# Performance work log

Hardware: AMD Instinct MI355X
Metric: run time of the kernel (lower is better)

The kernel has to match this reference:

```python
import jax, jax.numpy as jnp
import numpy as np

B, N, M, K = 2, 16384, 16384, 32
C_IN, C_OUT, KS = 64, 128, 15
RADIUS = 0.1
SIGMA = 0.5 * RADIUS  # module sets self.sigma = sigma * radius


def _generate_kernel_points(num_kpoints: int, radius: float) -> np.ndarray:
    # Fibonacci-sphere placement, matching the torch generate_kernel_points
    if num_kpoints == 1:
        return np.zeros((1, 3), dtype=np.float32)
    pts = np.zeros((num_kpoints, 3), dtype=np.float32)
    golden_angle = np.pi * (3 - np.sqrt(5))
    for i in range(num_kpoints):
        y = 1 - i / float(num_kpoints - 1) * 2
        r_y = np.sqrt(1 - y * y)
        theta = golden_angle * i
        pts[i] = np.array([np.cos(theta) * r_y, y, np.sin(theta) * r_y]) * radius
    return pts


def setup_inputs() -> dict:
    key = jax.random.key(0)
    k1, k2, k3, k4 = jax.random.split(key, 4)
    query_points = jax.random.uniform(k1, (B, N, 3), dtype=jnp.float32)
    support_points = jax.random.uniform(k2, (B, M, 3), dtype=jnp.float32)
    support_features = jax.random.normal(k3, (B, M, C_IN), dtype=jnp.float32)
    neighbor_idx = jax.random.randint(k4, (B, N, K), 0, M)
    kernel_points = jnp.asarray(_generate_kernel_points(KS, RADIUS * 0.8))
    k5 = jax.random.fold_in(key, 5)
    # kaiming-uniform-ish init on flattened (KS*C_IN, C_OUT)
    bound = np.sqrt(1.0 / (KS * C_IN))
    weights = jax.random.uniform(k5, (KS, C_IN, C_OUT), dtype=jnp.float32,
                                 minval=-bound, maxval=bound)
    bias = jnp.zeros((C_OUT,), dtype=jnp.float32)
    return {
        "query_points": query_points,
        "support_points": support_points,
        "support_features": support_features,
        "neighbor_idx": neighbor_idx,
        "kernel_points": kernel_points,
        "weights": weights,
        "bias": bias,
    }


def reference(query_points, support_points, support_features, neighbor_idx,
              kernel_points, weights, bias):
    # Batched gather: support[b, idx[b]] -> [B, N, K, *]
    gather = jax.vmap(lambda feats, idx: feats[idx])
    neighbor_points = gather(support_points, neighbor_idx)      # [B,N,K,3]
    neighbor_features = gather(support_features, neighbor_idx)  # [B,N,K,C_in]

    rel = neighbor_points - query_points[:, :, None, :]          # [B,N,K,3]
    # squared distance to each kernel point: [B,N,K,J]
    sq_dist = jnp.sum((rel[:, :, :, None, :] - kernel_points[None, None, None]) ** 2,
                      axis=-1)
    influences = jnp.exp(-sq_dist / (2 * SIGMA ** 2))
    influences = influences / (influences.sum(axis=-1, keepdims=True) + 1e-6)

    out = jnp.einsum('bnkc,bnkj,jco->bno', neighbor_features, influences, weights)
    return out + bias
```

## Files before the change

### kernel.cpp

```cpp
#include <hip/hip_runtime.h>
#include <hip/hip_bf16.h>


#define NB   16384
#define MB   16384
#define KN   32
#define CIN  64
#define COUT 128
#define KS   15
#define TP   32
#define FROW 1936

typedef __attribute__((ext_vector_type(8))) short short8;
typedef __attribute__((ext_vector_type(4))) float f32x4;

static __device__ __forceinline__ unsigned short f32_to_bf16_rne(float x) {
    unsigned int u = __float_as_uint(x);
    unsigned int lsb = (u >> 16) & 1u;
    u += 0x7fffu + lsb;
    return (unsigned short)(u >> 16);
}

__global__ __launch_bounds__(256)
void wfrag_prep(const float* __restrict__ Wg, unsigned short* __restrict__ wf) {
    const int tid = blockIdx.x * 256 + threadIdx.x;
    if (tid >= 30 * 8 * 64) return;
    const int l = tid & 63;
    const int t = (tid >> 6) & 7;
    const int s = tid >> 9;
    const int n  = t * 16 + (l & 15);
    const int kb = s * 32 + (l >> 4) * 8;
    short8 o;
    #pragma unroll
    for (int i = 0; i < 8; ++i)
        o[i] = (short)f32_to_bf16_rne(Wg[(kb + i) * COUT + n]);
    *(short8*)(wf + (size_t)tid * 8) = o;
}

__global__ __launch_bounds__(256)
void kpconv_mfma(const float* __restrict__ qp,
                 const float* __restrict__ sp,
                 const float* __restrict__ feats,
                 const int* __restrict__ nidx,
                 const float* __restrict__ kp,
                 const unsigned short* __restrict__ wfrag,
                 const float* __restrict__ bias,
                 float* __restrict__ out) {
    __shared__ __align__(16) char sF[TP * FROW];

    const int tid  = threadIdx.x;
    const int lane = tid & 63;
    const int wv   = tid >> 6;
    const int gp_base = blockIdx.x * TP;
    const int b = gp_base >> 14;
    const float* fb  = feats + (size_t)b * MB * CIN;
    const float* spb = sp + (size_t)b * MB * 3;

    const int n16  = lane & 15;
    const int quad = lane >> 4;

    const int jc = n16 < 14 ? n16 : 14;
    const float kxj = kp[3 * jc + 0];
    const float kyj = kp[3 * jc + 1];
    const float kzj = kp[3 * jc + 2];

    #pragma unroll 1
    for (int pt = 0; pt < 8; ++pt) {
        const int pl = wv * 8 + pt;
        const int gp = gp_base + pl;

        const int* ip = nidx + (size_t)gp * KN + quad * 8;
        int idxv[8];
        *(int4*)(&idxv[0]) = *(const int4*)(ip);
        *(int4*)(&idxv[4]) = *(const int4*)(ip + 4);

        const float qx = qp[3 * gp + 0];
        const float qy = qp[3 * gp + 1];
        const float qz = qp[3 * gp + 2];
        const float qkx = qx + kxj, qky = qy + kyj, qkz = qz + kzj;

        float e[8];
        #pragma unroll
        for (int i = 0; i < 8; ++i) {
            const float* s3 = spb + (size_t)idxv[i] * 3;
            const float dx = s3[0] - qkx;
            const float dy = s3[1] - qky;
            const float dz = s3[2] - qkz;
            const float d2 = fmaf(dx, dx, fmaf(dy, dy, dz * dz));
            float ev = __expf(-200.0f * d2);
            e[i] = (n16 < 15) ? ev : 0.0f;
        }

        short8 afrag;
        #pragma unroll
        for (int i = 0; i < 8; ++i) {
            float s = e[i];
            s += __shfl_xor(s, 1, 16);
            s += __shfl_xor(s, 2, 16);
            s += __shfl_xor(s, 4, 16);
            s += __shfl_xor(s, 8, 16);
            const float inv = __builtin_amdgcn_rcpf(s + 1e-6f);
            afrag[i] = (short)f32_to_bf16_rne(e[i] * inv);
        }

        short8 bfr[4];
        #pragma unroll
        for (int i = 0; i < 8; ++i) {
            const float* fr = fb + (size_t)idxv[i] * CIN + n16;
            #pragma unroll
            for (int t = 0; t < 4; ++t)
                bfr[t][i] = (short)f32_to_bf16_rne(fr[t * 16]);
        }

        f32x4 dd[4];
        #pragma unroll
        for (int t = 0; t < 4; ++t) {
            f32x4 z = {0.f, 0.f, 0.f, 0.f};
            dd[t] = __builtin_amdgcn_mfma_f32_16x16x32_bf16(afrag, bfr[t], z, 0, 0, 0);
        }

        unsigned short* fp_ = (unsigned short*)(sF + (size_t)pl * FROW);
        #pragma unroll
        for (int t = 0; t < 4; ++t) {
            #pragma unroll
            for (int r = 0; r < 4; ++r) {
                const int jr = quad * 4 + r;
                if (jr < 15)
                    fp_[jr * CIN + t * 16 + n16] = f32_to_bf16_rne(dd[t][r]);
            }
        }
    }
    __syncthreads();

    const int lm = lane & 15, lq = lane >> 4;
    const int t0 = 2 * wv, t1 = 2 * wv + 1;
    f32x4 acc00 = {0.f, 0.f, 0.f, 0.f};
    f32x4 acc01 = {0.f, 0.f, 0.f, 0.f};
    f32x4 acc10 = {0.f, 0.f, 0.f, 0.f};
    f32x4 acc11 = {0.f, 0.f, 0.f, 0.f};

    const char* a0p = sF + lm * FROW + lq * 16;
    const char* a1p = a0p + 16 * FROW;

    #pragma unroll 2
    for (int s = 0; s < 30; ++s) {
        const short8 a0 = *(const short8*)(a0p + s * 64);
        const short8 a1 = *(const short8*)(a1p + s * 64);
        const short8 b0 = *(const short8*)(wfrag + ((size_t)(s * 8 + t0) * 64 + lane) * 8);
        const short8 b1 = *(const short8*)(wfrag + ((size_t)(s * 8 + t1) * 64 + lane) * 8);
        acc00 = __builtin_amdgcn_mfma_f32_16x16x32_bf16(a0, b0, acc00, 0, 0, 0);
        acc01 = __builtin_amdgcn_mfma_f32_16x16x32_bf16(a0, b1, acc01, 0, 0, 0);
        acc10 = __builtin_amdgcn_mfma_f32_16x16x32_bf16(a1, b0, acc10, 0, 0, 0);
        acc11 = __builtin_amdgcn_mfma_f32_16x16x32_bf16(a1, b1, acc11, 0, 0, 0);
    }

    const float bs0 = bias[t0 * 16 + lm];
    const float bs1 = bias[t1 * 16 + lm];
    #pragma unroll
    for (int r = 0; r < 4; ++r) {
        const int pr0 = lq * 4 + r;
        const int pr1 = 16 + pr0;
        out[(size_t)(gp_base + pr0) * COUT + t0 * 16 + lm] = acc00[r] + bs0;
        out[(size_t)(gp_base + pr0) * COUT + t1 * 16 + lm] = acc01[r] + bs1;
        out[(size_t)(gp_base + pr1) * COUT + t0 * 16 + lm] = acc10[r] + bs0;
        out[(size_t)(gp_base + pr1) * COUT + t1 * 16 + lm] = acc11[r] + bs1;
    }
}

extern "C" void kernel_launch(void* const* d_in, const int* in_sizes, int n_in,
                              void* d_out, int out_size, void* d_ws, size_t ws_size,
                              hipStream_t stream) {
    const float* qp = (const float*)d_in[0];
    const float* sp = (const float*)d_in[1];
    const float* ft = (const float*)d_in[2];
    const int*   ni = (const int*)d_in[3];
    const float* kp = (const float*)d_in[4];
    const float* wg = (const float*)d_in[5];
    const float* bs = (const float*)d_in[6];
    float* o = (float*)d_out;

    unsigned short* wfrag = (unsigned short*)d_ws;

    hipLaunchKernelGGL(wfrag_prep, dim3(60), dim3(256), 0, stream, wg, wfrag);
    hipLaunchKernelGGL(kpconv_mfma, dim3((2 * NB) / TP), dim3(256), 0, stream,
                       qp, sp, ft, ni, kp, wfrag, bs, o);
}
```

Measured before the change: 130.7 us.

## Pre-convert features to bf16, use 512-thread blocks, swizzle LDS layout

Adds a prep pass that converts support features to packed bf16 in workspace, so the gather reads half the bytes. The main kernel moves to 512 threads (8 waves, 4 points each), swaps MFMA operand order so results pack as uint2 stores into an XOR-swizzled LDS layout, and gives each wave one output tile in the second GEMM. It also uses a cheaper round-half-up bf16 pack in place of RNE. The costs are an extra full pass over the features per call and bf16 gathers done as 2-byte scalar loads.

```diff
diff --git a/kernel.cpp b/kernel.cpp
--- a/kernel.cpp
+++ b/kernel.cpp
@@ -9,52 +9,80 @@
 #define COUT 128
 #define KS   15
 #define TP   32
-#define FROW 1936
+#define PROW 2064
+#define WFRAG_BYTES 245760u
+#define F16_BYTES   (2u * MB * CIN * 2u)
 
 typedef __attribute__((ext_vector_type(8))) short short8;
 typedef __attribute__((ext_vector_type(4))) float f32x4;
 
+static __device__ __forceinline__ unsigned int pack2_bf16(float f0, float f1) {
+    const unsigned int a = __float_as_uint(f0) + 0x8000u;
+    const unsigned int b = __float_as_uint(f1) + 0x8000u;
+    return (a >> 16) | (b & 0xffff0000u);
+}
+
+static __device__ __forceinline__ unsigned int pack2_bf16_rne(float f0, float f1) {
+    unsigned int a = __float_as_uint(f0);
+    unsigned int b = __float_as_uint(f1);
+    a += 0x7fffu + ((a >> 16) & 1u);
+    b += 0x7fffu + ((b >> 16) & 1u);
+    return (a >> 16) | (b & 0xffff0000u);
+}
+
 static __device__ __forceinline__ unsigned short f32_to_bf16_rne(float x) {
     unsigned int u = __float_as_uint(x);
-    unsigned int lsb = (u >> 16) & 1u;
-    u += 0x7fffu + lsb;
+    u += 0x7fffu + ((u >> 16) & 1u);
     return (unsigned short)(u >> 16);
 }
 
 __global__ __launch_bounds__(256)
-void wfrag_prep(const float* __restrict__ Wg, unsigned short* __restrict__ wf) {
-    const int tid = blockIdx.x * 256 + threadIdx.x;
-    if (tid >= 30 * 8 * 64) return;
-    const int l = tid & 63;
-    const int t = (tid >> 6) & 7;
-    const int s = tid >> 9;
-    const int n  = t * 16 + (l & 15);
-    const int kb = s * 32 + (l >> 4) * 8;
-    short8 o;
-    #pragma unroll
-    for (int i = 0; i < 8; ++i)
-        o[i] = (short)f32_to_bf16_rne(Wg[(kb + i) * COUT + n]);
-    *(short8*)(wf + (size_t)tid * 8) = o;
-}
-
-__global__ __launch_bounds__(256)
+void prep_kernel(const float* __restrict__ Wg, const float* __restrict__ feats,
+                 unsigned short* __restrict__ wf, unsigned int* __restrict__ f16,
+                 int do_feats) {
+    const int bid = blockIdx.x;
+    if (bid < 60) {
+        const int tid = bid * 256 + threadIdx.x;
+        const int l = tid & 63;
+        const int t = (tid >> 6) & 7;
+        const int s = tid >> 9;
+        const int n  = t * 16 + (l & 15);
+        const int kb = s * 32 + (l >> 4) * 8;
+        short8 o;
+        #pragma unroll
+        for (int i = 0; i < 8; ++i)
+            o[i] = (short)f32_to_bf16_rne(Wg[(kb + i) * COUT + n]);
+        *(short8*)(wf + (size_t)tid * 8) = o;
+    } else if (do_feats) {
+        const unsigned int t = (unsigned int)(bid - 60) * 256u + threadIdx.x;
+        if (t < 2u * MB * CIN / 2u) {
+            const float2 v = ((const float2*)feats)[t];
+            f16[t] = pack2_bf16_rne(v.x, v.y);
+        }
+    }
+}
+
+template<bool F16>
+__global__ __launch_bounds__(512, 4)
 void kpconv_mfma(const float* __restrict__ qp,
                  const float* __restrict__ sp,
                  const float* __restrict__ feats,
+                 const unsigned short* __restrict__ fbh16,
                  const int* __restrict__ nidx,
                  const float* __restrict__ kp,
                  const unsigned short* __restrict__ wfrag,
                  const float* __restrict__ bias,
                  float* __restrict__ out) {
-    __shared__ __align__(16) char sF[TP * FROW];
+    __shared__ __align__(16) char sF[TP * PROW];
 
     const int tid  = threadIdx.x;
     const int lane = tid & 63;
     const int wv   = tid >> 6;
     const int gp_base = blockIdx.x * TP;
     const int b = gp_base >> 14;
-    const float* fb  = feats + (size_t)b * MB * CIN;
-    const float* spb = sp + (size_t)b * MB * 3;
+    const float*          fbf = feats + (size_t)b * MB * CIN;
+    const unsigned short* fbh = fbh16 + (size_t)b * MB * CIN;
+    const float*          spb = sp + (size_t)b * MB * 3;
 
     const int n16  = lane & 15;
     const int quad = lane >> 4;
@@ -65,8 +93,8 @@
     const float kzj = kp[3 * jc + 2];
 
     #pragma unroll 1
-    for (int pt = 0; pt < 8; ++pt) {
-        const int pl = wv * 8 + pt;
+    for (int pt = 0; pt < 4; ++pt) {
+        const int pl = wv * 4 + pt;
         const int gp = gp_base + pl;
 
         const int* ip = nidx + (size_t)gp * KN + quad * 8;
@@ -87,11 +115,12 @@
             const float dy = s3[1] - qky;
             const float dz = s3[2] - qkz;
             const float d2 = fmaf(dx, dx, fmaf(dy, dy, dz * dz));
-            float ev = __expf(-200.0f * d2);
+            const float ev = __expf(-200.0f * d2);
             e[i] = (n16 < 15) ? ev : 0.0f;
         }
 
-        short8 afrag;
+        unsigned int iu[4];
+        float en[8];
         #pragma unroll
         for (int i = 0; i < 8; ++i) {
             float s = e[i];
@@ -99,71 +128,72 @@
             s += __shfl_xor(s, 2, 16);
             s += __shfl_xor(s, 4, 16);
             s += __shfl_xor(s, 8, 16);
-            const float inv = __builtin_amdgcn_rcpf(s + 1e-6f);
-            afrag[i] = (short)f32_to_bf16_rne(e[i] * inv);
-        }
-
-        short8 bfr[4];
-        #pragma unroll
-        for (int i = 0; i < 8; ++i) {
-            const float* fr = fb + (size_t)idxv[i] * CIN + n16;
-            #pragma unroll
-            for (int t = 0; t < 4; ++t)
-                bfr[t][i] = (short)f32_to_bf16_rne(fr[t * 16]);
-        }
-
-        f32x4 dd[4];
+            en[i] = e[i] * __builtin_amdgcn_rcpf(s + 1e-6f);
+        }
+        #pragma unroll
+        for (int ih = 0; ih < 4; ++ih)
+            iu[ih] = pack2_bf16(en[2 * ih], en[2 * ih + 1]);
+        const short8 ifrag = *(const short8*)iu;
+
+        unsigned int fu[4][4];
+        #pragma unroll
+        for (int ih = 0; ih < 4; ++ih) {
+            if (F16) {
+                const unsigned short* fr0 = fbh + (size_t)idxv[2 * ih]     * CIN + n16;
+                const unsigned short* fr1 = fbh + (size_t)idxv[2 * ih + 1] * CIN + n16;
+                #pragma unroll
+                for (int t = 0; t < 4; ++t) {
+                    const unsigned int lo = fr0[t * 16];
+                    const unsigned int hi = fr1[t * 16];
+                    fu[t][ih] = lo | (hi << 16);
+                }
+            } else {
+                const float* fr0 = fbf + (size_t)idxv[2 * ih]     * CIN + n16;
+                const float* fr1 = fbf + (size_t)idxv[2 * ih + 1] * CIN + n16;
+                #pragma unroll
+                for (int t = 0; t < 4; ++t)
+                    fu[t][ih] = pack2_bf16(fr0[t * 16], fr1[t * 16]);
+            }
+        }
+
         #pragma unroll
         for (int t = 0; t < 4; ++t) {
+            const short8 ffrag = *(const short8*)(fu[t]);
             f32x4 z = {0.f, 0.f, 0.f, 0.f};
-            dd[t] = __builtin_amdgcn_mfma_f32_16x16x32_bf16(afrag, bfr[t], z, 0, 0, 0);
-        }
-
-        unsigned short* fp_ = (unsigned short*)(sF + (size_t)pl * FROW);
-        #pragma unroll
-        for (int t = 0; t < 4; ++t) {
-            #pragma unroll
-            for (int r = 0; r < 4; ++r) {
-                const int jr = quad * 4 + r;
-                if (jr < 15)
-                    fp_[jr * CIN + t * 16 + n16] = f32_to_bf16_rne(dd[t][r]);
-            }
+            const f32x4 dd = __builtin_amdgcn_mfma_f32_16x16x32_bf16(ffrag, ifrag, z, 0, 0, 0);
+            const unsigned int lo = pack2_bf16(dd[0], dd[1]);
+            const unsigned int hi = pack2_bf16(dd[2], dd[3]);
+            const int off = pl * PROW + n16 * 128 +
+                            ((t * 32 + quad * 8) ^ ((n16 & 7) << 4));
+            uint2 v; v.x = lo; v.y = hi;
+            *(uint2*)(sF + off) = v;
         }
     }
     __syncthreads();
 
-    const int lm = lane & 15, lq = lane >> 4;
-    const int t0 = 2 * wv, t1 = 2 * wv + 1;
-    f32x4 acc00 = {0.f, 0.f, 0.f, 0.f};
-    f32x4 acc01 = {0.f, 0.f, 0.f, 0.f};
-    f32x4 acc10 = {0.f, 0.f, 0.f, 0.f};
-    f32x4 acc11 = {0.f, 0.f, 0.f, 0.f};
-
-    const char* a0p = sF + lm * FROW + lq * 16;
-    const char* a1p = a0p + 16 * FROW;
-
-    #pragma unroll 2
+    const int lm = n16;
+    f32x4 acc0 = {0.f, 0.f, 0.f, 0.f};
+    f32x4 acc1 = {0.f, 0.f, 0.f, 0.f};
+    const char* aBase = sF + lm * PROW;
+
+    #pragma unroll
     for (int s = 0; s < 30; ++s) {
-        const short8 a0 = *(const short8*)(a0p + s * 64);
-        const short8 a1 = *(const short8*)(a1p + s * 64);
-        const short8 b0 = *(const short8*)(wfrag + ((size_t)(s * 8 + t0) * 64 + lane) * 8);
-        const short8 b1 = *(const short8*)(wfrag + ((size_t)(s * 8 + t1) * 64 + lane) * 8);
-        acc00 = __builtin_amdgcn_mfma_f32_16x16x32_bf16(a0, b0, acc00, 0, 0, 0);
-        acc01 = __builtin_amdgcn_mfma_f32_16x16x32_bf16(a0, b1, acc01, 0, 0, 0);
-        acc10 = __builtin_amdgcn_mfma_f32_16x16x32_bf16(a1, b0, acc10, 0, 0, 0);
-        acc11 = __builtin_amdgcn_mfma_f32_16x16x32_bf16(a1, b1, acc11, 0, 0, 0);
-    }
-
-    const float bs0 = bias[t0 * 16 + lm];
-    const float bs1 = bias[t1 * 16 + lm];
+        const int j   = s >> 1;
+        const int c0b = (s & 1) * 64 + quad * 16;
+        const int off = j * 128 + (c0b ^ ((j & 7) << 4));
+        const short8 a0 = *(const short8*)(aBase + off);
+        const short8 a1 = *(const short8*)(aBase + 16 * PROW + off);
+        const short8 bf = *(const short8*)(wfrag + ((size_t)(s * 8 + wv) * 64 + lane) * 8);
+        acc0 = __builtin_amdgcn_mfma_f32_16x16x32_bf16(a0, bf, acc0, 0, 0, 0);
+        acc1 = __builtin_amdgcn_mfma_f32_16x16x32_bf16(a1, bf, acc1, 0, 0, 0);
+    }
+
+    const float bsv = bias[wv * 16 + lm];
     #pragma unroll
     for (int r = 0; r < 4; ++r) {
-        const int pr0 = lq * 4 + r;
-        const int pr1 = 16 + pr0;
-        out[(size_t)(gp_base + pr0) * COUT + t0 * 16 + lm] = acc00[r] + bs0;
-        out[(size_t)(gp_base + pr0) * COUT + t1 * 16 + lm] = acc01[r] + bs1;
-        out[(size_t)(gp_base + pr1) * COUT + t0 * 16 + lm] = acc10[r] + bs0;
-        out[(size_t)(gp_base + pr1) * COUT + t1 * 16 + lm] = acc11[r] + bs1;
+        const int pr = quad * 4 + r;
+        out[(size_t)(gp_base + pr)      * COUT + wv * 16 + lm] = acc0[r] + bsv;
+        out[(size_t)(gp_base + 16 + pr) * COUT + wv * 16 + lm] = acc1[r] + bsv;
     }
 }
 
@@ -180,8 +210,18 @@
     float* o = (float*)d_out;
 
     unsigned short* wfrag = (unsigned short*)d_ws;
-
-    hipLaunchKernelGGL(wfrag_prep, dim3(60), dim3(256), 0, stream, wg, wfrag);
-    hipLaunchKernelGGL(kpconv_mfma, dim3((2 * NB) / TP), dim3(256), 0, stream,
-                       qp, sp, ft, ni, kp, wfrag, bs, o);
-}
+    unsigned int*   f16   = (unsigned int*)((char*)d_ws + WFRAG_BYTES);
+    const int do_feats = (ws_size >= (size_t)WFRAG_BYTES + F16_BYTES) ? 1 : 0;
+
+    const int prep_blocks = do_feats ? (60 + 4096) : 60;
+    hipLaunchKernelGGL(prep_kernel, dim3(prep_blocks), dim3(256), 0, stream,
+                       wg, ft, wfrag, f16, do_feats);
+
+    if (do_feats) {
+        hipLaunchKernelGGL((kpconv_mfma<true>), dim3((2 * NB) / TP), dim3(512), 0, stream,
+                           qp, sp, ft, (const unsigned short*)f16, ni, kp, wfrag, bs, o);
+    } else {
+        hipLaunchKernelGGL((kpconv_mfma<false>), dim3((2 * NB) / TP), dim3(512), 0, stream,
+                           qp, sp, ft, (const unsigned short*)f16, ni, kp, wfrag, bs, o);
+    }
+}
```

Measured after the change: 112.6 us. 13.9% less time.
